# Optimization experiments

Measured on AMD Instinct MI355X. Metric: run time of the kernel, lower is better.

Reference implementation:

```python
import jax, jax.numpy as jnp
import numpy as np

N = 100000      # nodes
E = 2500000     # edges
DIN, H, DOUT = 3, 32, 4
EPS = 1e-5

def _lin(k, i, o):
    kw, kb = jax.random.split(k)
    lim = 1.0 / np.sqrt(i)
    W = jax.random.uniform(kw, (i, o), jnp.float32, -lim, lim)
    b = jax.random.uniform(kb, (o,), jnp.float32, -lim, lim)
    return W, b

def setup_inputs():
    key = jax.random.key(0)
    ks = jax.random.split(key, 12)
    x = jax.random.normal(ks[0], (N, DIN), jnp.float32)
    edge_index = jax.random.randint(ks[1], (2, E), 0, N, dtype=jnp.int32)
    w_in1, b_in1 = _lin(ks[2], DIN, H)
    w_in2, b_in2 = _lin(ks[3], H, H)
    gamma = jnp.ones((H,), jnp.float32)
    beta = jnp.zeros((H,), jnp.float32)
    wg1, bg1 = _lin(ks[4], H, H)
    wg2, bg2 = _lin(ks[5], H, H)
    wg3, bg3 = _lin(ks[6], H, H)
    wo1, bo1 = _lin(ks[7], H, H)
    wo2, bo2 = _lin(ks[8], H, H)
    wo3, bo3 = _lin(ks[9], H, DOUT)
    return dict(x=x, w_in1=w_in1, b_in1=b_in1, w_in2=w_in2, b_in2=b_in2,
                gamma=gamma, beta=beta,
                wg1=wg1, bg1=bg1, wg2=wg2, bg2=bg2, wg3=wg3, bg3=bg3,
                wo1=wo1, bo1=bo1, wo2=wo2, bo2=bo2, wo3=wo3, bo3=bo3,
                edge_index=edge_index)

def _gcn(h, W, b, src, dst, norm):
    # PyG GCNConv: x' = scatter_add(norm * (xW)[src] -> dst) + bias
    hw = h @ W                                   # [N, H]
    msg = hw[src] * norm[:, None]                # [E+N, H] gather + scale
    out = jax.ops.segment_sum(msg, dst, num_segments=N)
    return out + b

def reference(x, w_in1, b_in1, w_in2, b_in2, gamma, beta,
              wg1, bg1, wg2, bg2, wg3, bg3,
              wo1, bo1, wo2, bo2, wo3, bo3, edge_index):
    leaky = lambda v: jax.nn.leaky_relu(v, 0.01)
    # input MLP
    h = leaky(x @ w_in1 + b_in1)
    h = leaky(h @ w_in2 + b_in2)
    # BatchNorm1d (training-mode batch statistics, biased variance)
    mu = jnp.mean(h, axis=0)
    var = jnp.mean((h - mu) ** 2, axis=0)
    h = (h - mu) * jax.lax.rsqrt(var + EPS) * gamma + beta
    # gcn_norm with self-loops: deg over target index, sym normalization
    loop = jnp.arange(N, dtype=edge_index.dtype)
    src = jnp.concatenate([edge_index[0], loop])
    dst = jnp.concatenate([edge_index[1], loop])
    deg = jax.ops.segment_sum(jnp.ones_like(src, jnp.float32), dst, num_segments=N)
    dis = jax.lax.rsqrt(deg)                     # deg >= 1 due to self-loops
    norm = dis[src] * dis[dst]                   # [E+N]
    h = jax.nn.elu(_gcn(h, wg1, bg1, src, dst, norm))
    h = jax.nn.elu(_gcn(h, wg2, bg2, src, dst, norm))
    h = jax.nn.elu(_gcn(h, wg3, bg3, src, dst, norm))
    # output MLP
    r = leaky(h @ wo1 + bo1)
    r = leaky(r @ wo2 + bo2)
    r = r @ wo3 + bo3                            # [N, 4]
    r = r.at[:, 0].set(jax.nn.sigmoid(r[:, 0]))
    return r
```

## Files before the change

kernel.cpp:

```cpp
#include <hip/hip_runtime.h>
#include <hip/hip_fp16.h>

#define HF 32
#define EPS 1e-5f
#define BSH 8
#define BSZ 256
#define CH  4096
#define SUBCAP 1024
#define CAP (8*SUBCAP)

__device__ __forceinline__ float leaky(float v){ return fmaxf(v, 0.01f*v); }
__device__ __forceinline__ float elu1(float v){ return v > 0.f ? v : (expf(v)-1.f); }
__device__ __forceinline__ float sigmoidf(float v){ return 1.f/(1.f+expf(-v)); }

__device__ __forceinline__ void addrow8(float* a, float4 v){
    const __half2* p = (const __half2*)&v;
#pragma unroll
    for (int k = 0; k < 4; k++){
        float2 f = __half22float2(p[k]);
        a[2*k] += f.x; a[2*k+1] += f.y;
    }
}
__device__ __forceinline__ float4 h2add4f(float4 a, float4 b){
    __half2* pa = (__half2*)&a; __half2* pb = (__half2*)&b;
    float4 r; __half2* pr = (__half2*)&r;
#pragma unroll
    for (int k = 0; k < 4; k++) pr[k] = __hadd2(pa[k], pb[k]);
    return r;
}

__global__ __launch_bounds__(256)
void k_mlp(const float* __restrict__ x,
           const float* __restrict__ w1, const float* __restrict__ b1,
           const float* __restrict__ w2, const float* __restrict__ b2,
           __half* __restrict__ h, float* __restrict__ stats, int N){
    __shared__ float sW1[3*HF], sB1[HF], sW2[HF*HF], sB2[HF];
    __shared__ float sh[256][33];
    int t = threadIdx.x;
    for (int i = t; i < 3*HF; i += 256) sW1[i] = w1[i];
    if (t < HF){ sB1[t] = b1[t]; sB2[t] = b2[t]; }
    for (int i = t; i < HF*HF; i += 256) sW2[i] = w2[i];
    __syncthreads();
    int n = blockIdx.x*256 + t;
    float h2[HF];
    if (n < N){
        float x0 = x[(size_t)n*3], x1 = x[(size_t)n*3+1], x2 = x[(size_t)n*3+2];
        float h1[HF];
#pragma unroll
        for (int j = 0; j < HF; j++){
            float v = fmaf(x0, sW1[j], fmaf(x1, sW1[HF+j], fmaf(x2, sW1[2*HF+j], sB1[j])));
            h1[j] = leaky(v);
        }
#pragma unroll
        for (int j = 0; j < HF; j++){
            float v = sB2[j];
#pragma unroll
            for (int i = 0; i < HF; i++) v = fmaf(h1[i], sW2[i*HF+j], v);
            h2[j] = leaky(v);
        }
        float4* hv = (float4*)(h + (size_t)n*HF);
#pragma unroll
        for (int jb = 0; jb < 4; jb++){
            __half2 hh[4];
#pragma unroll
            for (int k = 0; k < 4; k++)
                hh[k] = __float22half2_rn(make_float2(h2[jb*8+2*k], h2[jb*8+2*k+1]));
            hv[jb] = *(float4*)hh;
        }
    } else {
#pragma unroll
        for (int j = 0; j < HF; j++) h2[j] = 0.f;
    }
#pragma unroll
    for (int j = 0; j < HF; j++) sh[t][j] = h2[j];
    __syncthreads();
    int f = t & 31, g = t >> 5;
    float s = 0.f, ss = 0.f;
    for (int i = 0; i < 32; i++){
        float v = sh[g*32 + i][f];
        s += v; ss += v*v;
    }
    __syncthreads();
    sh[g][f] = s; sh[8+g][f] = ss;
    __syncthreads();
    if (t < HF){
        float a = 0.f, b = 0.f;
#pragma unroll
        for (int g2 = 0; g2 < 8; g2++){ a += sh[g2][t]; b += sh[8+g2][t]; }
        atomicAdd(&stats[t], a);
        atomicAdd(&stats[HF+t], b);
    }
}

__global__ __launch_bounds__(256)
void k_bin(const int* __restrict__ src, const int* __restrict__ dst,
           int* __restrict__ gfill, int* __restrict__ ep, int E, int B){
    __shared__ int lcnt[512], lbase[512], lpos[512];
    int t = threadIdx.x;
    for (int i = t; i < B; i += 256){ lcnt[i] = 0; lpos[i] = 0; }
    __syncthreads();
    int base = blockIdx.x * CH;
    int xcd = blockIdx.x & 7;
#pragma unroll
    for (int i = 0; i < CH/1024; i++){
        int e = base + t + i*1024;
        int d0 = (e       < E) ? dst[e]       : -1;
        int d1 = (e+256   < E) ? dst[e+256]   : -1;
        int d2 = (e+512   < E) ? dst[e+512]   : -1;
        int d3 = (e+768   < E) ? dst[e+768]   : -1;
        if (d0 >= 0) atomicAdd(&lcnt[d0 >> BSH], 1);
        if (d1 >= 0) atomicAdd(&lcnt[d1 >> BSH], 1);
        if (d2 >= 0) atomicAdd(&lcnt[d2 >> BSH], 1);
        if (d3 >= 0) atomicAdd(&lcnt[d3 >> BSH], 1);
    }
    __syncthreads();
    for (int i = t; i < B; i += 256){
        int c = lcnt[i];
        lbase[i] = c ? (i*CAP + xcd*SUBCAP + atomicAdd(&gfill[i*8 + xcd], c)) : 0;
    }
    __syncthreads();
#pragma unroll
    for (int i = 0; i < CH/1024; i++){
        int e = base + t + i*1024;
#pragma unroll
        for (int k = 0; k < 4; k++){
            int ee = e + k*256;
            if (ee < E){
                int d = dst[ee], s = src[ee];
                int b = d >> BSH;
                int p = lbase[b] + atomicAdd(&lpos[b], 1);
                ep[p] = (s << BSH) | (d & (BSZ-1));
            }
        }
    }
}

__global__ __launch_bounds__(256)
void k_bucketD(int* __restrict__ ep, const int* __restrict__ gfill,
               int2* __restrict__ rowp2, float* __restrict__ dis, int N, int B){
    __shared__ int sep[CAP];
    __shared__ int lcnt[256], lpre[256], lfill[256], sc[256];
    int b = blockIdx.x, t = threadIdx.x;
    int cx[8], coff[8], cnt = 0;
#pragma unroll
    for (int x = 0; x < 8; x++){ cx[x] = gfill[b*8 + x]; coff[x] = cnt; cnt += cx[x]; }
    lcnt[t] = 0; lfill[t] = 0;
    __syncthreads();
    int base = b*CAP;
#pragma unroll
    for (int x = 0; x < 8; x++)
        for (int j = t; j < cx[x]; j += 256) sep[coff[x] + j] = ep[base + x*SUBCAP + j];
    __syncthreads();
    for (int e = t; e < cnt; e += 256) atomicAdd(&lcnt[sep[e] & (BSZ-1)], 1);
    __syncthreads();
    int v = lcnt[t];
    sc[t] = v; __syncthreads();
    for (int off = 1; off < 256; off <<= 1){
        int u = (t >= off) ? sc[t - off] : 0;
        __syncthreads();
        sc[t] += u;
        __syncthreads();
    }
    int pre = sc[t] - v;
    lpre[t] = pre;
    int n = b*BSZ + t;
    if (n < N){
        rowp2[n] = make_int2(base + pre, base + pre + v);
        dis[n]   = rsqrtf((float)(v + 1));
    }
    __syncthreads();
    for (int e = t; e < cnt; e += 256){
        int val = sep[e];
        int d = val & (BSZ-1);
        int p = lpre[d] + atomicAdd(&lfill[d], 1);
        ep[base + p] = val >> BSH;
    }
}

__global__ __launch_bounds__(256)
void k_bn_t1(const __half* __restrict__ h, const float* __restrict__ stats,
             const float* __restrict__ gamma, const float* __restrict__ beta,
             const float* __restrict__ W, const float* __restrict__ dis,
             __half* __restrict__ tout, int N){
    __shared__ float sW[HF*HF];
    __shared__ float sh[64][33];
    int tid = threadIdx.x;
    for (int i = tid; i < HF*HF; i += 256) sW[i] = W[i];
    int nib = tid >> 2, l = tid & 3;
    int n = blockIdx.x*64 + nib;
    float hv[8];
    float d = 0.f;
    if (n < N){
        float4 raw = ((const float4*)h)[(size_t)n*4 + l];
        const __half2* p = (const __half2*)&raw;
        float tmp[8];
#pragma unroll
        for (int k = 0; k < 4; k++){
            float2 f2 = __half22float2(p[k]);
            tmp[2*k] = f2.x; tmp[2*k+1] = f2.y;
        }
        d = dis[n];
        float inv = 1.0f / (float)N;
#pragma unroll
        for (int c = 0; c < 8; c++){
            int f = 8*l + c;
            float mu  = stats[f]    * inv;
            float var = stats[HF+f] * inv - mu*mu;
            float rs  = rsqrtf(var + EPS);
            hv[c] = (tmp[c] - mu) * rs * gamma[f] + beta[f];
        }
    } else {
#pragma unroll
        for (int c = 0; c < 8; c++) hv[c] = 0.f;
    }
    __syncthreads();
#pragma unroll
    for (int c = 0; c < 8; c++) sh[nib][8*l + c] = hv[c];
    __syncthreads();
    float o[8] = {0.f,0.f,0.f,0.f,0.f,0.f,0.f,0.f};
#pragma unroll
    for (int i = 0; i < HF; i++){
        float hvv = sh[nib][i];
        float4 w0 = *(const float4*)&sW[i*HF + 8*l];
        float4 w1 = *(const float4*)&sW[i*HF + 8*l + 4];
        o[0] = fmaf(hvv, w0.x, o[0]); o[1] = fmaf(hvv, w0.y, o[1]);
        o[2] = fmaf(hvv, w0.z, o[2]); o[3] = fmaf(hvv, w0.w, o[3]);
        o[4] = fmaf(hvv, w1.x, o[4]); o[5] = fmaf(hvv, w1.y, o[5]);
        o[6] = fmaf(hvv, w1.z, o[6]); o[7] = fmaf(hvv, w1.w, o[7]);
    }
    if (n < N){
        __half2 hh[4];
#pragma unroll
        for (int k = 0; k < 4; k++)
            hh[k] = __float22half2_rn(make_float2(o[2*k]*d, o[2*k+1]*d));
        ((float4*)tout)[(size_t)n*4 + l] = *(float4*)hh;
    }
}

__global__ __launch_bounds__(256)
void k_gather_t(const __half* __restrict__ tin, const int* __restrict__ esrc,
                const int2* __restrict__ rowp2, const float* __restrict__ dis,
                const float* __restrict__ bias, const float* __restrict__ W,
                __half* __restrict__ tout, int N){
    __shared__ float sW[HF*HF];
    __shared__ float sh[64][33];
    int tid = threadIdx.x;
    for (int i = tid; i < HF*HF; i += 256) sW[i] = W[i];
    int nib = tid >> 2, l = tid & 3;
    int n = blockIdx.x*64 + nib;
    float acc[8] = {0.f,0.f,0.f,0.f,0.f,0.f,0.f,0.f};
    float d = 0.f;
    const float4* tv = (const float4*)tin;
    if (n < N){
        addrow8(acc, tv[(size_t)n*4 + l]);
        int2 r = rowp2[n];
        int e = r.x, e1 = r.y;
        while (e < e1 && (e & 3)){ addrow8(acc, tv[(size_t)esrc[e]*4 + l]); e++; }
        for (; e + 3 < e1; e += 4){
            int4 s4 = *(const int4*)&esrc[e];
            float4 v0 = tv[(size_t)s4.x*4 + l];
            float4 v1 = tv[(size_t)s4.y*4 + l];
            float4 v2 = tv[(size_t)s4.z*4 + l];
            float4 v3 = tv[(size_t)s4.w*4 + l];
            addrow8(acc, h2add4f(h2add4f(v0, v1), h2add4f(v2, v3)));
        }
        for (; e < e1; e++) addrow8(acc, tv[(size_t)esrc[e]*4 + l]);
        d = dis[n];
#pragma unroll
        for (int c = 0; c < 8; c++)
            acc[c] = elu1(fmaf(d, acc[c], bias[8*l + c]));
    }
    __syncthreads();
#pragma unroll
    for (int c = 0; c < 8; c++) sh[nib][8*l + c] = acc[c];
    __syncthreads();
    float o[8] = {0.f,0.f,0.f,0.f,0.f,0.f,0.f,0.f};
#pragma unroll
    for (int i = 0; i < HF; i++){
        float hvv = sh[nib][i];
        float4 w0 = *(const float4*)&sW[i*HF + 8*l];
        float4 w1 = *(const float4*)&sW[i*HF + 8*l + 4];
        o[0] = fmaf(hvv, w0.x, o[0]); o[1] = fmaf(hvv, w0.y, o[1]);
        o[2] = fmaf(hvv, w0.z, o[2]); o[3] = fmaf(hvv, w0.w, o[3]);
        o[4] = fmaf(hvv, w1.x, o[4]); o[5] = fmaf(hvv, w1.y, o[5]);
        o[6] = fmaf(hvv, w1.z, o[6]); o[7] = fmaf(hvv, w1.w, o[7]);
    }
    if (n < N){
        __half2 hh[4];
#pragma unroll
        for (int k = 0; k < 4; k++)
            hh[k] = __float22half2_rn(make_float2(o[2*k]*d, o[2*k+1]*d));
        ((float4*)tout)[(size_t)n*4 + l] = *(float4*)hh;
    }
}

__global__ __launch_bounds__(256)
void k_gather_out(const __half* __restrict__ tin, const int* __restrict__ esrc,
                  const int2* __restrict__ rowp2, const float* __restrict__ dis,
                  const float* __restrict__ bg3,
                  const float* __restrict__ wo1, const float* __restrict__ bo1,
                  const float* __restrict__ wo2, const float* __restrict__ bo2,
                  const float* __restrict__ wo3, const float* __restrict__ bo3,
                  float* __restrict__ out, int N){
    __shared__ float sW1[HF*HF], sW2[HF*HF], sW3[HF*4];
    __shared__ float sh[64][33], sh2[64][33];
    int tid = threadIdx.x;
    for (int i = tid; i < HF*HF; i += 256){ sW1[i] = wo1[i]; sW2[i] = wo2[i]; }
    if (tid < HF*4) sW3[tid] = wo3[tid];
    int nib = tid >> 2, l = tid & 3;
    int n = blockIdx.x*64 + nib;
    float acc[8] = {0.f,0.f,0.f,0.f,0.f,0.f,0.f,0.f};
    const float4* tv = (const float4*)tin;
    if (n < N){
        addrow8(acc, tv[(size_t)n*4 + l]);
        int2 r = rowp2[n];
        int e = r.x, e1 = r.y;
        while (e < e1 && (e & 3)){ addrow8(acc, tv[(size_t)esrc[e]*4 + l]); e++; }
        for (; e + 3 < e1; e += 4){
            int4 s4 = *(const int4*)&esrc[e];
            float4 v0 = tv[(size_t)s4.x*4 + l];
            float4 v1 = tv[(size_t)s4.y*4 + l];
            float4 v2 = tv[(size_t)s4.z*4 + l];
            float4 v3 = tv[(size_t)s4.w*4 + l];
            addrow8(acc, h2add4f(h2add4f(v0, v1), h2add4f(v2, v3)));
        }
        for (; e < e1; e++) addrow8(acc, tv[(size_t)esrc[e]*4 + l]);
        float d = dis[n];
#pragma unroll
        for (int c = 0; c < 8; c++)
            acc[c] = elu1(fmaf(d, acc[c], bg3[8*l + c]));
    }
    __syncthreads();
#pragma unroll
    for (int c = 0; c < 8; c++) sh[nib][8*l + c] = acc[c];
    __syncthreads();
    float o1[8];
#pragma unroll
    for (int c = 0; c < 8; c++) o1[c] = bo1[8*l + c];
#pragma unroll
    for (int i = 0; i < HF; i++){
        float hvv = sh[nib][i];
        float4 w0 = *(const float4*)&sW1[i*HF + 8*l];
        float4 w1 = *(const float4*)&sW1[i*HF + 8*l + 4];
        o1[0] = fmaf(hvv, w0.x, o1[0]); o1[1] = fmaf(hvv, w0.y, o1[1]);
        o1[2] = fmaf(hvv, w0.z, o1[2]); o1[3] = fmaf(hvv, w0.w, o1[3]);
        o1[4] = fmaf(hvv, w1.x, o1[4]); o1[5] = fmaf(hvv, w1.y, o1[5]);
        o1[6] = fmaf(hvv, w1.z, o1[6]); o1[7] = fmaf(hvv, w1.w, o1[7]);
    }
#pragma unroll
    for (int c = 0; c < 8; c++) sh2[nib][8*l + c] = leaky(o1[c]);
    __syncthreads();
    float o2[8];
#pragma unroll
    for (int c = 0; c < 8; c++) o2[c] = bo2[8*l + c];
#pragma unroll
    for (int i = 0; i < HF; i++){
        float hvv = sh2[nib][i];
        float4 w0 = *(const float4*)&sW2[i*HF + 8*l];
        float4 w1 = *(const float4*)&sW2[i*HF + 8*l + 4];
        o2[0] = fmaf(hvv, w0.x, o2[0]); o2[1] = fmaf(hvv, w0.y, o2[1]);
        o2[2] = fmaf(hvv, w0.z, o2[2]); o2[3] = fmaf(hvv, w0.w, o2[3]);
        o2[4] = fmaf(hvv, w1.x, o2[4]); o2[5] = fmaf(hvv, w1.y, o2[5]);
        o2[6] = fmaf(hvv, w1.z, o2[6]); o2[7] = fmaf(hvv, w1.w, o2[7]);
    }
#pragma unroll
    for (int c = 0; c < 8; c++) sh[nib][8*l + c] = leaky(o2[c]);
    __syncthreads();
    if (n < N){
        float v = bo3[l];
#pragma unroll
        for (int i = 0; i < HF; i++) v = fmaf(sh[nib][i], sW3[i*4 + l], v);
        if (l == 0) v = sigmoidf(v);
        out[(size_t)n*4 + l] = v;
    }
}

extern "C" void kernel_launch(void* const* d_in, const int* in_sizes, int n_in,
                              void* d_out, int out_size, void* d_ws, size_t ws_size,
                              hipStream_t stream) {
    const float* x     = (const float*)d_in[0];
    const float* w_in1 = (const float*)d_in[1];
    const float* b_in1 = (const float*)d_in[2];
    const float* w_in2 = (const float*)d_in[3];
    const float* b_in2 = (const float*)d_in[4];
    const float* gamma = (const float*)d_in[5];
    const float* beta  = (const float*)d_in[6];
    const float* wg1   = (const float*)d_in[7];
    const float* bg1   = (const float*)d_in[8];
    const float* wg2   = (const float*)d_in[9];
    const float* bg2   = (const float*)d_in[10];
    const float* wg3   = (const float*)d_in[11];
    const float* bg3   = (const float*)d_in[12];
    const float* wo1   = (const float*)d_in[13];
    const float* bo1   = (const float*)d_in[14];
    const float* wo2   = (const float*)d_in[15];
    const float* bo2   = (const float*)d_in[16];
    const float* wo3   = (const float*)d_in[17];
    const float* bo3   = (const float*)d_in[18];
    const int*   ei    = (const int*)d_in[19];

    int N = in_sizes[0] / 3;
    int E = in_sizes[19] / 2;
    int B = (N + BSZ - 1) >> BSH;

    char* w = (char*)d_ws;
    size_t o = 0;
    auto alloc = [&](size_t bytes){ size_t r = o; o = (o + bytes + 255) & ~(size_t)255; return r; };
    float* stats = (float*)(w + alloc(2*HF*sizeof(float)));
    int*   gfill = (int*)  (w + alloc((size_t)B*8*4));
    size_t zero_bytes = o;
    int2*  rowp2 = (int2*) (w + alloc((size_t)N*8));
    float* dis   = (float*)(w + alloc((size_t)N*4));
    int*   ep    = (int*)  (w + alloc((size_t)B*CAP*4));
    __half* bufH = (__half*)(w + alloc((size_t)N*HF*2));
    __half* tA   = (__half*)(w + alloc((size_t)N*HF*2));
    __half* tB   = (__half*)(w + alloc((size_t)N*HF*2));

    hipMemsetAsync(d_ws, 0, zero_bytes, stream);

    const int* src = ei;
    const int* dst = ei + E;
    int NB1 = (N + 255) / 256;
    int NC  = (E + CH - 1) / CH;
    int GB  = (N + 63) / 64;

    k_mlp    <<<NB1, 256, 0, stream>>>(x, w_in1, b_in1, w_in2, b_in2, bufH, stats, N);
    k_bin    <<<NC,  256, 0, stream>>>(src, dst, gfill, ep, E, B);
    k_bucketD<<<B,   256, 0, stream>>>(ep, gfill, rowp2, dis, N, B);

    k_bn_t1   <<<GB, 256, 0, stream>>>(bufH, stats, gamma, beta, wg1, dis, tA, N);
    k_gather_t<<<GB, 256, 0, stream>>>(tA, ep, rowp2, dis, bg1, wg2, tB, N);
    k_gather_t<<<GB, 256, 0, stream>>>(tB, ep, rowp2, dis, bg2, wg3, tA, N);
    k_gather_out<<<GB, 256, 0, stream>>>(tA, ep, rowp2, dis, bg3,
                                         wo1, bo1, wo2, bo2, wo3, bo3, (float*)d_out, N);
}
```

Baseline: 314.6 us.

## Fuse MLP and edge binning launches, add nontemporal hints and wider gather unroll

Merges the input MLP kernel and the edge-binning kernel into one launch that splits work by block index over a shared-memory union, so the two independent stages run concurrently. The binning path now keeps src/dst values in registers instead of reloading them. Edge lists and intermediate feature rows get nontemporal loads and stores. The gather loops process 8 neighbours per iteration to put more loads in flight. This adds register pressure and possible cache-policy side effects on data that is reused.

Measured after the change: 380.1 us. 20.8% more time.

```diff
diff --git a/kernel.cpp b/kernel.cpp
--- a/kernel.cpp
+++ b/kernel.cpp
@@ -9,10 +9,22 @@
 #define SUBCAP 1024
 #define CAP (8*SUBCAP)
 
+typedef int   vi4 __attribute__((ext_vector_type(4)));
+typedef float vf4 __attribute__((ext_vector_type(4)));
+
 __device__ __forceinline__ float leaky(float v){ return fmaxf(v, 0.01f*v); }
 __device__ __forceinline__ float elu1(float v){ return v > 0.f ? v : (expf(v)-1.f); }
 __device__ __forceinline__ float sigmoidf(float v){ return 1.f/(1.f+expf(-v)); }
 
+__device__ __forceinline__ int4 nt_load_i4(const int* p){
+    vi4 v = __builtin_nontemporal_load((const vi4*)p);
+    return make_int4(v.x, v.y, v.z, v.w);
+}
+__device__ __forceinline__ void nt_store_f4(float4 v, float4* p){
+    vf4 t; t.x = v.x; t.y = v.y; t.z = v.z; t.w = v.w;
+    __builtin_nontemporal_store(t, (vf4*)p);
+}
+
 __device__ __forceinline__ void addrow8(float* a, float4 v){
     const __half2* p = (const __half2*)&v;
 #pragma unroll
@@ -29,107 +41,107 @@
     return r;
 }
 
+union SMem {
+    struct {
+        float sW1[3*HF]; float sB1[HF]; float sW2[HF*HF]; float sB2[HF];
+        float sh[256][33];
+    } mlp;
+    struct { int lcnt[512]; int lbase[512]; int lpos[512]; } bin;
+};
+
 __global__ __launch_bounds__(256)
-void k_mlp(const float* __restrict__ x,
-           const float* __restrict__ w1, const float* __restrict__ b1,
-           const float* __restrict__ w2, const float* __restrict__ b2,
-           __half* __restrict__ h, float* __restrict__ stats, int N){
-    __shared__ float sW1[3*HF], sB1[HF], sW2[HF*HF], sB2[HF];
-    __shared__ float sh[256][33];
+void k_mlp_bin(const float* __restrict__ x,
+               const float* __restrict__ w1, const float* __restrict__ b1,
+               const float* __restrict__ w2, const float* __restrict__ b2,
+               __half* __restrict__ h, float* __restrict__ stats,
+               const int* __restrict__ src, const int* __restrict__ dst,
+               int* __restrict__ gfill, int* __restrict__ ep,
+               int N, int E, int B, int NB1){
+    __shared__ SMem sm;
     int t = threadIdx.x;
-    for (int i = t; i < 3*HF; i += 256) sW1[i] = w1[i];
-    if (t < HF){ sB1[t] = b1[t]; sB2[t] = b2[t]; }
-    for (int i = t; i < HF*HF; i += 256) sW2[i] = w2[i];
-    __syncthreads();
-    int n = blockIdx.x*256 + t;
-    float h2[HF];
-    if (n < N){
-        float x0 = x[(size_t)n*3], x1 = x[(size_t)n*3+1], x2 = x[(size_t)n*3+2];
-        float h1[HF];
-#pragma unroll
-        for (int j = 0; j < HF; j++){
-            float v = fmaf(x0, sW1[j], fmaf(x1, sW1[HF+j], fmaf(x2, sW1[2*HF+j], sB1[j])));
-            h1[j] = leaky(v);
-        }
-#pragma unroll
-        for (int j = 0; j < HF; j++){
-            float v = sB2[j];
-#pragma unroll
-            for (int i = 0; i < HF; i++) v = fmaf(h1[i], sW2[i*HF+j], v);
-            h2[j] = leaky(v);
-        }
-        float4* hv = (float4*)(h + (size_t)n*HF);
-#pragma unroll
-        for (int jb = 0; jb < 4; jb++){
-            __half2 hh[4];
-#pragma unroll
-            for (int k = 0; k < 4; k++)
-                hh[k] = __float22half2_rn(make_float2(h2[jb*8+2*k], h2[jb*8+2*k+1]));
-            hv[jb] = *(float4*)hh;
+    if ((int)blockIdx.x < NB1){
+        for (int i = t; i < 3*HF; i += 256) sm.mlp.sW1[i] = w1[i];
+        if (t < HF){ sm.mlp.sB1[t] = b1[t]; sm.mlp.sB2[t] = b2[t]; }
+        for (int i = t; i < HF*HF; i += 256) sm.mlp.sW2[i] = w2[i];
+        __syncthreads();
+        int n = blockIdx.x*256 + t;
+        float h2[HF];
+        if (n < N){
+            float x0 = x[(size_t)n*3], x1 = x[(size_t)n*3+1], x2 = x[(size_t)n*3+2];
+            float h1[HF];
+#pragma unroll
+            for (int j = 0; j < HF; j++){
+                float v = fmaf(x0, sm.mlp.sW1[j], fmaf(x1, sm.mlp.sW1[HF+j],
+                          fmaf(x2, sm.mlp.sW1[2*HF+j], sm.mlp.sB1[j])));
+                h1[j] = leaky(v);
+            }
+#pragma unroll
+            for (int j = 0; j < HF; j++){
+                float v = sm.mlp.sB2[j];
+#pragma unroll
+                for (int i = 0; i < HF; i++) v = fmaf(h1[i], sm.mlp.sW2[i*HF+j], v);
+                h2[j] = leaky(v);
+            }
+            float4* hv = (float4*)(h + (size_t)n*HF);
+#pragma unroll
+            for (int jb = 0; jb < 4; jb++){
+                __half2 hh[4];
+#pragma unroll
+                for (int k = 0; k < 4; k++)
+                    hh[k] = __float22half2_rn(make_float2(h2[jb*8+2*k], h2[jb*8+2*k+1]));
+                hv[jb] = *(float4*)hh;
+            }
+        } else {
+#pragma unroll
+            for (int j = 0; j < HF; j++) h2[j] = 0.f;
+        }
+#pragma unroll
+        for (int j = 0; j < HF; j++) sm.mlp.sh[t][j] = h2[j];
+        __syncthreads();
+        int f = t & 31, g = t >> 5;
+        float s = 0.f, ss = 0.f;
+        for (int i = 0; i < 32; i++){
+            float v = sm.mlp.sh[g*32 + i][f];
+            s += v; ss += v*v;
+        }
+        __syncthreads();
+        sm.mlp.sh[g][f] = s; sm.mlp.sh[8+g][f] = ss;
+        __syncthreads();
+        if (t < HF){
+            float a = 0.f, b = 0.f;
+#pragma unroll
+            for (int g2 = 0; g2 < 8; g2++){ a += sm.mlp.sh[g2][t]; b += sm.mlp.sh[8+g2][t]; }
+            atomicAdd(&stats[t], a);
+            atomicAdd(&stats[HF+t], b);
         }
     } else {
-#pragma unroll
-        for (int j = 0; j < HF; j++) h2[j] = 0.f;
-    }
-#pragma unroll
-    for (int j = 0; j < HF; j++) sh[t][j] = h2[j];
-    __syncthreads();
-    int f = t & 31, g = t >> 5;
-    float s = 0.f, ss = 0.f;
-    for (int i = 0; i < 32; i++){
-        float v = sh[g*32 + i][f];
-        s += v; ss += v*v;
-    }
-    __syncthreads();
-    sh[g][f] = s; sh[8+g][f] = ss;
-    __syncthreads();
-    if (t < HF){
-        float a = 0.f, b = 0.f;
-#pragma unroll
-        for (int g2 = 0; g2 < 8; g2++){ a += sh[g2][t]; b += sh[8+g2][t]; }
-        atomicAdd(&stats[t], a);
-        atomicAdd(&stats[HF+t], b);
-    }
-}
-
-__global__ __launch_bounds__(256)
-void k_bin(const int* __restrict__ src, const int* __restrict__ dst,
-           int* __restrict__ gfill, int* __restrict__ ep, int E, int B){
-    __shared__ int lcnt[512], lbase[512], lpos[512];
-    int t = threadIdx.x;
-    for (int i = t; i < B; i += 256){ lcnt[i] = 0; lpos[i] = 0; }
-    __syncthreads();
-    int base = blockIdx.x * CH;
-    int xcd = blockIdx.x & 7;
-#pragma unroll
-    for (int i = 0; i < CH/1024; i++){
-        int e = base + t + i*1024;
-        int d0 = (e       < E) ? dst[e]       : -1;
-        int d1 = (e+256   < E) ? dst[e+256]   : -1;
-        int d2 = (e+512   < E) ? dst[e+512]   : -1;
-        int d3 = (e+768   < E) ? dst[e+768]   : -1;
-        if (d0 >= 0) atomicAdd(&lcnt[d0 >> BSH], 1);
-        if (d1 >= 0) atomicAdd(&lcnt[d1 >> BSH], 1);
-        if (d2 >= 0) atomicAdd(&lcnt[d2 >> BSH], 1);
-        if (d3 >= 0) atomicAdd(&lcnt[d3 >> BSH], 1);
-    }
-    __syncthreads();
-    for (int i = t; i < B; i += 256){
-        int c = lcnt[i];
-        lbase[i] = c ? (i*CAP + xcd*SUBCAP + atomicAdd(&gfill[i*8 + xcd], c)) : 0;
-    }
-    __syncthreads();
-#pragma unroll
-    for (int i = 0; i < CH/1024; i++){
-        int e = base + t + i*1024;
-#pragma unroll
-        for (int k = 0; k < 4; k++){
-            int ee = e + k*256;
-            if (ee < E){
-                int d = dst[ee], s = src[ee];
-                int b = d >> BSH;
-                int p = lbase[b] + atomicAdd(&lpos[b], 1);
-                ep[p] = (s << BSH) | (d & (BSZ-1));
+        int bid = blockIdx.x - NB1;
+        for (int i = t; i < B; i += 256){ sm.bin.lcnt[i] = 0; sm.bin.lpos[i] = 0; }
+        __syncthreads();
+        int base = bid * CH;
+        int xcd = blockIdx.x & 7;
+        int dv[16], sv[16];
+#pragma unroll
+        for (int i = 0; i < 16; i++){
+            int e = base + t + i*256;
+            dv[i] = (e < E) ? __builtin_nontemporal_load(&dst[e]) : -1;
+            sv[i] = (e < E) ? __builtin_nontemporal_load(&src[e]) : 0;
+        }
+#pragma unroll
+        for (int i = 0; i < 16; i++)
+            if (dv[i] >= 0) atomicAdd(&sm.bin.lcnt[dv[i] >> BSH], 1);
+        __syncthreads();
+        for (int i = t; i < B; i += 256){
+            int c = sm.bin.lcnt[i];
+            sm.bin.lbase[i] = c ? (i*CAP + xcd*SUBCAP + atomicAdd(&gfill[i*8 + xcd], c)) : 0;
+        }
+        __syncthreads();
+#pragma unroll
+        for (int i = 0; i < 16; i++){
+            if (dv[i] >= 0){
+                int d = dv[i], bb = d >> BSH;
+                int p = sm.bin.lbase[bb] + atomicAdd(&sm.bin.lpos[bb], 1);
+                __builtin_nontemporal_store((sv[i] << BSH) | (d & (BSZ-1)), &ep[p]);
             }
         }
     }
@@ -149,7 +161,8 @@
     int base = b*CAP;
 #pragma unroll
     for (int x = 0; x < 8; x++)
-        for (int j = t; j < cx[x]; j += 256) sep[coff[x] + j] = ep[base + x*SUBCAP + j];
+        for (int j = t; j < cx[x]; j += 256)
+            sep[coff[x] + j] = __builtin_nontemporal_load(&ep[base + x*SUBCAP + j]);
     __syncthreads();
     for (int e = t; e < cnt; e += 256) atomicAdd(&lcnt[sep[e] & (BSZ-1)], 1);
     __syncthreads();
@@ -173,7 +186,7 @@
         int val = sep[e];
         int d = val & (BSZ-1);
         int p = lpre[d] + atomicAdd(&lfill[d], 1);
-        ep[base + p] = val >> BSH;
+        __builtin_nontemporal_store(val >> BSH, &ep[base + p]);
     }
 }
 
@@ -256,8 +269,22 @@
         int2 r = rowp2[n];
         int e = r.x, e1 = r.y;
         while (e < e1 && (e & 3)){ addrow8(acc, tv[(size_t)esrc[e]*4 + l]); e++; }
+        for (; e + 7 < e1; e += 8){
+            int4 a4 = nt_load_i4(&esrc[e]);
+            int4 b4 = nt_load_i4(&esrc[e+4]);
+            float4 v0 = tv[(size_t)a4.x*4 + l];
+            float4 v1 = tv[(size_t)a4.y*4 + l];
+            float4 v2 = tv[(size_t)a4.z*4 + l];
+            float4 v3 = tv[(size_t)a4.w*4 + l];
+            float4 v4 = tv[(size_t)b4.x*4 + l];
+            float4 v5 = tv[(size_t)b4.y*4 + l];
+            float4 v6 = tv[(size_t)b4.z*4 + l];
+            float4 v7 = tv[(size_t)b4.w*4 + l];
+            addrow8(acc, h2add4f(h2add4f(v0, v1), h2add4f(v2, v3)));
+            addrow8(acc, h2add4f(h2add4f(v4, v5), h2add4f(v6, v7)));
+        }
         for (; e + 3 < e1; e += 4){
-            int4 s4 = *(const int4*)&esrc[e];
+            int4 s4 = nt_load_i4(&esrc[e]);
             float4 v0 = tv[(size_t)s4.x*4 + l];
             float4 v1 = tv[(size_t)s4.y*4 + l];
             float4 v2 = tv[(size_t)s4.z*4 + l];
@@ -290,7 +317,7 @@
 #pragma unroll
         for (int k = 0; k < 4; k++)
             hh[k] = __float22half2_rn(make_float2(o[2*k]*d, o[2*k+1]*d));
-        ((float4*)tout)[(size_t)n*4 + l] = *(float4*)hh;
+        nt_store_f4(*(float4*)hh, &((float4*)tout)[(size_t)n*4 + l]);
     }
 }
 
@@ -316,8 +343,22 @@
         int2 r = rowp2[n];
         int e = r.x, e1 = r.y;
         while (e < e1 && (e & 3)){ addrow8(acc, tv[(size_t)esrc[e]*4 + l]); e++; }
+        for (; e + 7 < e1; e += 8){
+            int4 a4 = nt_load_i4(&esrc[e]);
+            int4 b4 = nt_load_i4(&esrc[e+4]);
+            float4 v0 = tv[(size_t)a4.x*4 + l];
+            float4 v1 = tv[(size_t)a4.y*4 + l];
+            float4 v2 = tv[(size_t)a4.z*4 + l];
+            float4 v3 = tv[(size_t)a4.w*4 + l];
+            float4 v4 = tv[(size_t)b4.x*4 + l];
+            float4 v5 = tv[(size_t)b4.y*4 + l];
+            float4 v6 = tv[(size_t)b4.z*4 + l];
+            float4 v7 = tv[(size_t)b4.w*4 + l];
+            addrow8(acc, h2add4f(h2add4f(v0, v1), h2add4f(v2, v3)));
+            addrow8(acc, h2add4f(h2add4f(v4, v5), h2add4f(v6, v7)));
+        }
         for (; e + 3 < e1; e += 4){
-            int4 s4 = *(const int4*)&esrc[e];
+            int4 s4 = nt_load_i4(&esrc[e]);
             float4 v0 = tv[(size_t)s4.x*4 + l];
             float4 v1 = tv[(size_t)s4.y*4 + l];
             float4 v2 = tv[(size_t)s4.z*4 + l];
@@ -424,9 +465,9 @@
     int NC  = (E + CH - 1) / CH;
     int GB  = (N + 63) / 64;
 
-    k_mlp    <<<NB1, 256, 0, stream>>>(x, w_in1, b_in1, w_in2, b_in2, bufH, stats, N);
-    k_bin    <<<NC,  256, 0, stream>>>(src, dst, gfill, ep, E, B);
-    k_bucketD<<<B,   256, 0, stream>>>(ep, gfill, rowp2, dis, N, B);
+    k_mlp_bin<<<NB1 + NC, 256, 0, stream>>>(x, w_in1, b_in1, w_in2, b_in2, bufH, stats,
+                                            src, dst, gfill, ep, N, E, B, NB1);
+    k_bucketD<<<B, 256, 0, stream>>>(ep, gfill, rowp2, dis, N, B);
 
     k_bn_t1   <<<GB, 256, 0, stream>>>(bufH, stats, gamma, beta, wg1, dis, tA, N);
     k_gather_t<<<GB, 256, 0, stream>>>(tA, ep, rowp2, dis, bg1, wg2, tB, N);
```
